# Optimization experiments

Measured on AMD Instinct MI355X. Metric: run time of the kernel, lower is better.

The kernel has to match this reference:

```python
import jax, jax.numpy as jnp
import numpy as np

B, D, K = 32, 400, 200
H = 8            # kernel_size (GRU hidden)
LAYERS = 4
OUT = 8


def setup_inputs() -> dict:
    key = jax.random.key(0)
    ks = jax.random.split(key, 16)
    x = jax.random.normal(ks[0], (B, D, K), dtype=jnp.float32)
    # variable-length zero padding along time per (b, k) sequence
    lengths = jax.random.randint(ks[1], (B, K), D // 2, D + 1)
    tmask = jnp.arange(D)[None, :, None] < lengths[:, None, :]   # (B, D, K)
    x = x * tmask
    s = 1.0 / np.sqrt(H)
    def u(k, shape):
        return jax.random.uniform(k, shape, jnp.float32, -s, s)
    return {
        "x": x,
        "w_ih0": u(ks[2], (2, 3 * H, 1)),
        "w_hh0": u(ks[3], (2, 3 * H, H)),
        "b_ih0": u(ks[4], (2, 3 * H)),
        "b_hh0": u(ks[5], (2, 3 * H)),
        "w_ih": u(ks[6], (LAYERS - 1, 2, 3 * H, 2 * H)),
        "w_hh": u(ks[7], (LAYERS - 1, 2, 3 * H, H)),
        "b_ih": u(ks[8], (LAYERS - 1, 2, 3 * H)),
        "b_hh": u(ks[9], (LAYERS - 1, 2, 3 * H)),
        "lin1_w": u(ks[10], (H, 2 * H)),
        "lin1_b": u(ks[11], (H,)),
        "lin2_w": u(ks[12], (OUT, H)),
        "lin2_b": u(ks[13], (OUT,)),
    }


def _gru_dir(x, mask, Wih, Whh, bih, bhh):
    # x: (N, T, in), mask: (N, T) bool -> (N, T, H); zero past each length
    gi = jnp.einsum('nti,gi->tng', x, Wih) + bih          # (T, N, 3H) input gates
    m = mask.T[:, :, None]                                 # (T, N, 1)
    h0 = jnp.zeros((x.shape[0], Whh.shape[1]), x.dtype)
    def step(h, inp):
        gi_t, m_t = inp
        gh = h @ Whh.T + bhh
        ir, iz, inn = jnp.split(gi_t, 3, axis=-1)          # PyTorch gate order r, z, n
        hr, hz, hn = jnp.split(gh, 3, axis=-1)
        r = jax.nn.sigmoid(ir + hr)
        z = jax.nn.sigmoid(iz + hz)
        n = jnp.tanh(inn + r * hn)
        h = jnp.where(m_t, (1.0 - z) * n + z * h, h)
        return h, jnp.where(m_t, h, 0.0)
    _, out = jax.lax.scan(step, h0, (gi, m))
    return out.transpose(1, 0, 2)


def _bidir_gru(x, mask, rev_idx, p):
    Wih, Whh, bih, bhh = p
    fwd = _gru_dir(x, mask, Wih[0], Whh[0], bih[0], bhh[0])
    # backward dir of a packed sequence: reverse within each valid region
    x_rev = jnp.take_along_axis(x, rev_idx[:, :, None], axis=1)
    bwd_rev = _gru_dir(x_rev, mask, Wih[1], Whh[1], bih[1], bhh[1])
    bwd = jnp.take_along_axis(bwd_rev, rev_idx[:, :, None], axis=1)
    bwd = jnp.where(mask[:, :, None], bwd, 0.0)
    return jnp.concatenate([fwd, bwd], axis=-1)


def _forward(x, w_ih0, w_hh0, b_ih0, b_hh0, w_ih, w_hh, b_ih, b_hh,
             lin1_w, lin1_b, lin2_w, lin2_b):
    b, d, k = x.shape
    seq = x.transpose(0, 2, 1).reshape(b * k, d, 1)         # (N, T, 1)
    vals = seq[:, :, 0]
    zm = vals == 0.0
    lengths = jnp.where(zm.any(axis=1), jnp.argmax(zm, axis=1), d)  # (N,)
    mask = jnp.arange(d)[None, :] < lengths[:, None]        # (N, T)
    rev_idx = jnp.clip(lengths[:, None] - 1 - jnp.arange(d)[None, :], 0, d - 1)
    h = _bidir_gru(seq, mask, rev_idx, (w_ih0, w_hh0, b_ih0, b_hh0))
    for l in range(w_ih.shape[0]):                          # layers 1..3
        h = _bidir_gru(h, mask, rev_idx, (w_ih[l], w_hh[l], b_ih[l], b_hh[l]))
    # last valid timestep per sequence (matches argmax-of-all-zero gather)
    last = jnp.take_along_axis(h, (lengths - 1)[:, None, None], axis=1)[:, 0, :]
    feat = last.reshape(b, k, -1)                           # (B, K, 2H)
    y = jax.nn.leaky_relu(feat @ lin1_w.T + lin1_b, negative_slope=0.2)
    return y @ lin2_w.T + lin2_b                            # (B, K, OUT)


def reference(x, w_ih0, w_hh0, b_ih0, b_hh0, w_ih, w_hh, b_ih, b_hh,
              lin1_w, lin1_b, lin2_w, lin2_b):
    return _forward(x, w_ih0, w_hh0, b_ih0, b_hh0, w_ih, w_hh, b_ih, b_hh,
                    lin1_w, lin1_b, lin2_w, lin2_b)
```

## Files before the change

kernel.cpp:

```cpp
#include <hip/hip_runtime.h>

#define BB 32
#define DD 400
#define KK 200
#define NN (BB*KK)
#define NBINS 512
#define NSIMD 1024

typedef _Float16 half_t;
typedef _Float16 f16x2 __attribute__((ext_vector_type(2)));

__device__ __forceinline__ float dot2(f16x2 w, f16x2 v, float acc) {
  return __builtin_amdgcn_fdot2(w, v, acc, false);
}
__device__ __forceinline__ f16x2 bc16(int v) { return __builtin_bit_cast(f16x2, v); }
__device__ __forceinline__ int pkh(float a, float b) {
  return __builtin_bit_cast(int, __builtin_amdgcn_cvt_pkrtz(a, b));
}

__device__ __forceinline__ float fast_sigmoid(float x) {
  float e = __builtin_amdgcn_exp2f(-1.4426950408889634f * x);
  return __builtin_amdgcn_rcpf(1.0f + e);
}
__device__ __forceinline__ float fast_tanh(float x) {
  float e = __builtin_amdgcn_exp2f(-2.8853900817779268f * x);
  return 2.0f * __builtin_amdgcn_rcpf(1.0f + e) - 1.0f;
}

#define QPERMI(v, P) __builtin_amdgcn_mov_dpp((v), (P)*0x55, 0xF, 0xF, true)
#define HMIRROR(v) __int_as_float(__builtin_amdgcn_mov_dpp(__float_as_int(v), 0x141, 0xF, 0xF, true))

__global__ __launch_bounds__(256) void transpose_x(const float* __restrict__ x,
                                                   float* __restrict__ xt) {
  __shared__ float tile[32][33];
  int b = blockIdx.x, t0 = blockIdx.y * 32, k0 = blockIdx.z * 32;
  int tx = threadIdx.x, ty = threadIdx.y;
#pragma unroll
  for (int i = 0; i < 32; i += 8) {
    int t = t0 + ty + i, k = k0 + tx;
    tile[ty + i][tx] = (t < DD && k < KK) ? x[((size_t)b * DD + t) * KK + k] : 0.0f;
  }
  __syncthreads();
#pragma unroll
  for (int i = 0; i < 32; i += 8) {
    int k = k0 + ty + i, t = t0 + tx;
    if (k < KK && t < DD) xt[((size_t)b * KK + k) * DD + t] = tile[tx][ty + i];
  }
}

__global__ __launch_bounds__(64) void compute_lengths(const float* __restrict__ xt,
                                                      int* __restrict__ lengths,
                                                      int* __restrict__ hist) {
  int n = blockIdx.x, lane = threadIdx.x;
  int m = DD;
  for (int t = lane; t < DD; t += 64) {
    if (xt[(size_t)n * DD + t] == 0.0f) { m = t; break; }
  }
#pragma unroll
  for (int off = 1; off < 64; off <<= 1) {
    int o = __shfl_xor(m, off, 64);
    m = (o < m) ? o : m;
  }
  if (lane == 0) {
    lengths[n] = m;
    atomicAdd(&hist[m], 1);
  }
}

__global__ __launch_bounds__(64) void scan_offsets(const int* __restrict__ hist,
                                                   int* __restrict__ offs) {
  int lane = threadIdx.x;
  int v[8], tot = 0;
#pragma unroll
  for (int i = 0; i < 8; ++i) { v[i] = tot; tot += hist[lane * 8 + i]; }
  int incl = tot;
#pragma unroll
  for (int off = 1; off < 64; off <<= 1) {
    int oth = __shfl_up(incl, off, 64);
    if (lane >= off) incl += oth;
  }
  int excl = incl - tot;
#pragma unroll
  for (int i = 0; i < 8; ++i) offs[lane * 8 + i] = excl + v[i];
}

__global__ __launch_bounds__(256) void scatter_sort(const int* __restrict__ lengths,
                                                    int* __restrict__ offs,
                                                    int* __restrict__ order,
                                                    int* __restrict__ len_sorted) {
  int n = blockIdx.x * 256 + threadIdx.x;
  if (n >= NN) return;
  int len = lengths[n];
  int pos = atomicAdd(&offs[len], 1);
  order[pos] = n;
  len_sorted[pos] = len;
}

__device__ __forceinline__ int octet_of_wave(int p, int W) {
  int E = W - NSIMD;
  if (E <= 0) return W - 1 - p;
  if (p >= NSIMD) return p - NSIMD;
  if (p >= E) return W - 1 - (p - E);
  return (W - 1 - NSIMD + E) - p;
}


template <int IN_DIM, bool IND_IN, bool WRITE_SEQ, bool FWD_ONLY>
__global__ __attribute__((amdgpu_waves_per_eu(2, 2))) __launch_bounds__(64)
void gru_scan(
    const void* __restrict__ in, half_t* __restrict__ out, float* __restrict__ feat,
    const int* __restrict__ len_sorted, const int* __restrict__ order,
    const float* __restrict__ Wih, const float* __restrict__ Whh,
    const float* __restrict__ bih, const float* __restrict__ bhh, int nseq) {
  int p = blockIdx.x;
  int lane = threadIdx.x & 63;
  int G = FWD_ONLY ? nseq : nseq * 2;
  int W = (G + 7) >> 3;
  if (p >= W) return;
  int o = octet_of_wave(p, W);
  int gidx = o * 8 + (lane >> 3);
  int li = lane & 7;
  if (gidx >= G) return;
  int sg  = FWD_ONLY ? gidx : (gidx >> 1);
  int dir = FWD_ONLY ? 0 : (gidx & 1);
  int len = len_sorted[sg];

  int qb = li & 4;
  int wp[3][4];
  f16x2 wi2[3][8];
  float wi1[3];
  float bs[3], bh2;
#pragma unroll
  for (int gt = 0; gt < 3; ++gt) {
    int row = dir * 24 + gt * 8 + li;
    if constexpr (IN_DIM == 16) {
#pragma unroll
      for (int q = 0; q < 8; ++q) {
        f16x2 w;
        w.x = (half_t)Wih[row * 16 + 2 * q];
        w.y = (half_t)Wih[row * 16 + 2 * q + 1];
        wi2[gt][q] = w;
      }
    } else {
      wi1[gt] = Wih[row];
    }
#pragma unroll
    for (int P = 0; P < 4; ++P)
      wp[gt][P] = pkh(Whh[row * 8 + qb + P], Whh[row * 8 + ((qb + P) ^ 7)]);
    bs[gt] = bih[row] + ((gt < 2) ? bhh[row] : 0.0f);
    if (gt == 2) bh2 = bhh[row];
  }

  int steps = len;
  float h = 0.0f;

  const float* px = nullptr;
  const half_t* pxh = nullptr;
  ptrdiff_t xstep;
  if constexpr (IN_DIM == 1) {
    const float* basep = (const float*)in + (IND_IN ? (size_t)order[sg] * DD : (size_t)sg * DD);
    px = basep + ((dir == 0) ? 0 : (len - 1));
    xstep = (dir == 0) ? 1 : -1;
  } else {
    const half_t* basep = (const half_t*)in + (size_t)(sg >> 2) * DD * 64 + (sg & 3) * 8;
    pxh = basep + (size_t)((dir == 0) ? 0 : (len - 1)) * 64;
    xstep = (dir == 0) ? 64 : -64;
  }

  half_t* pw = nullptr; ptrdiff_t wstep = 0;
  if constexpr (WRITE_SEQ) {
    pw = out + ((size_t)(sg >> 2) * DD + ((dir == 0) ? 0 : (len - 1))) * 64
             + dir * 32 + (sg & 3) * 8 + li;
    wstep = (dir == 0) ? 64 : -64;
  }

  auto core = [&](float a0, float a1, float a2) {
    float hm = HMIRROR(h);
    int hp = pkh(h, hm);
    f16x2 u0 = bc16(QPERMI(hp, 0));
    f16x2 u1 = bc16(QPERMI(hp, 1));
    f16x2 u2 = bc16(QPERMI(hp, 2));
    f16x2 u3 = bc16(QPERMI(hp, 3));

    float c0 = dot2(bc16(wp[0][3]), u3, dot2(bc16(wp[0][2]), u2,
               dot2(bc16(wp[0][1]), u1, dot2(bc16(wp[0][0]), u0, a0))));
    float c1 = dot2(bc16(wp[1][3]), u3, dot2(bc16(wp[1][2]), u2,
               dot2(bc16(wp[1][1]), u1, dot2(bc16(wp[1][0]), u0, a1))));
    float c2 = dot2(bc16(wp[2][3]), u3, dot2(bc16(wp[2][2]), u2,
               dot2(bc16(wp[2][1]), u1, dot2(bc16(wp[2][0]), u0, bh2))));

    float r = fast_sigmoid(c0);
    float z = fast_sigmoid(c1);
    float n = fast_tanh(a2 + r * c2);
    h = z * (h - n) + n;
    if constexpr (WRITE_SEQ) { *pw = (half_t)h; pw += wstep; }
  };

  if constexpr (IN_DIM == 1) {
    float s0_, s1_, s2_, s3_;
    auto ld = [&](float& S_) { S_ = *px; px += xstep; };
    auto st = [&](float& S_, bool pf) {
      float a0 = fmaf(wi1[0], S_, bs[0]);
      float a1 = fmaf(wi1[1], S_, bs[1]);
      float a2 = fmaf(wi1[2], S_, bs[2]);
      if (pf) ld(S_);
      core(a0, a1, a2);
    };
    ld(s0_); ld(s1_); ld(s2_); ld(s3_);
    int t = 0;
    for (; t + 4 <= steps; t += 4) {
      st(s0_, true); st(s1_, true); st(s2_, true); st(s3_, true);
    }
    int rem = steps - t;
    if (rem > 0) st(s0_, false);
    if (rem > 1) st(s1_, false);
    if (rem > 2) st(s2_, false);
  } else {
    uint4 b0_[2], b1_[2], b2_[2], b3_[2];
    auto ld = [&](uint4 (&B_)[2]) {
      const uint4* q4 = reinterpret_cast<const uint4*>(pxh);
      B_[0] = q4[0]; B_[1] = q4[4];
      pxh += xstep;
    };
    auto st = [&](uint4 (&B_)[2], bool pf) {
      float a0 = bs[0], a1 = bs[1], a2 = bs[2];
#pragma unroll
      for (int q = 0; q < 2; ++q) {
        f16x2 p0 = __builtin_bit_cast(f16x2, B_[q].x);
        f16x2 p1 = __builtin_bit_cast(f16x2, B_[q].y);
        f16x2 p2 = __builtin_bit_cast(f16x2, B_[q].z);
        f16x2 p3 = __builtin_bit_cast(f16x2, B_[q].w);
        a0 = dot2(wi2[0][4*q], p0, a0); a0 = dot2(wi2[0][4*q+1], p1, a0);
        a0 = dot2(wi2[0][4*q+2], p2, a0); a0 = dot2(wi2[0][4*q+3], p3, a0);
        a1 = dot2(wi2[1][4*q], p0, a1); a1 = dot2(wi2[1][4*q+1], p1, a1);
        a1 = dot2(wi2[1][4*q+2], p2, a1); a1 = dot2(wi2[1][4*q+3], p3, a1);
        a2 = dot2(wi2[2][4*q], p0, a2); a2 = dot2(wi2[2][4*q+1], p1, a2);
        a2 = dot2(wi2[2][4*q+2], p2, a2); a2 = dot2(wi2[2][4*q+3], p3, a2);
      }
      if (pf) ld(B_);
      core(a0, a1, a2);
    };
    ld(b0_); ld(b1_); ld(b2_); ld(b3_);
    int t = 0;
    for (; t + 4 <= steps; t += 4) {
      st(b0_, true); st(b1_, true); st(b2_, true); st(b3_, true);
    }
    int rem = steps - t;
    if (rem > 0) st(b0_, false);
    if (rem > 1) st(b1_, false);
    if (rem > 2) st(b2_, false);
  }

  if constexpr (!WRITE_SEQ) {
    feat[(size_t)order[sg] * 16 + dir * 8 + li] = h;
  }
}

__global__ __launch_bounds__(256) void bwd_last(
    const half_t* __restrict__ in, float* __restrict__ feat,
    const int* __restrict__ len_sorted, const int* __restrict__ order,
    const float* __restrict__ Wih, const float* __restrict__ bih,
    const float* __restrict__ bhh, int nseq) {
  int tid = blockIdx.x * blockDim.x + threadIdx.x;
  int sg = tid >> 3, li = tid & 7;
  if (sg >= nseq) return;
  int len = len_sorted[sg];
  const half_t* xp = in + ((size_t)(sg >> 2) * DD + (len - 1)) * 64 + (sg & 3) * 8;
  float xv[16];
#pragma unroll
  for (int j = 0; j < 8; ++j) { xv[j] = (float)xp[j]; xv[8 + j] = (float)xp[32 + j]; }
  float a[3], bh[3];
#pragma unroll
  for (int gt = 0; gt < 3; ++gt) {
    int row = 24 + gt * 8 + li;
    const float* wpp = Wih + row * 16;
    float acc = bih[row];
#pragma unroll
    for (int j = 0; j < 16; ++j) acc = fmaf(wpp[j], xv[j], acc);
    a[gt] = acc;
    bh[gt] = bhh[row];
  }
  float r = fast_sigmoid(a[0] + bh[0]);
  float z = fast_sigmoid(a[1] + bh[1]);
  float n = fast_tanh(a[2] + r * bh[2]);
  float h = (1.0f - z) * n;
  feat[(size_t)order[sg] * 16 + 8 + li] = h;
}

__global__ __launch_bounds__(256) void head_kernel(
    const float* __restrict__ feat, const float* __restrict__ w1,
    const float* __restrict__ b1, const float* __restrict__ w2,
    const float* __restrict__ b2, float* __restrict__ out) {
  int n = blockIdx.x * blockDim.x + threadIdx.x;
  if (n >= NN) return;
  float f[16];
  const float4* p = reinterpret_cast<const float4*>(feat + (size_t)n * 16);
#pragma unroll
  for (int q = 0; q < 4; ++q) {
    float4 v = p[q];
    f[4*q] = v.x; f[4*q+1] = v.y; f[4*q+2] = v.z; f[4*q+3] = v.w;
  }
  float y[8];
#pragma unroll
  for (int o = 0; o < 8; ++o) {
    float s = b1[o];
#pragma unroll
    for (int j = 0; j < 16; ++j) s += f[j] * w1[o * 16 + j];
    y[o] = (s > 0.0f) ? s : 0.2f * s;
  }
#pragma unroll
  for (int o2 = 0; o2 < 8; ++o2) {
    float s = b2[o2];
#pragma unroll
    for (int o = 0; o < 8; ++o) s += y[o] * w2[o2 * 8 + o];
    out[(size_t)n * 8 + o2] = s;
  }
}

extern "C" void kernel_launch(void* const* d_in, const int* in_sizes, int n_in,
                              void* d_out, int out_size, void* d_ws, size_t ws_size,
                              hipStream_t stream) {
  const float* x      = (const float*)d_in[0];
  const float* w_ih0  = (const float*)d_in[1];
  const float* w_hh0  = (const float*)d_in[2];
  const float* b_ih0  = (const float*)d_in[3];
  const float* b_hh0  = (const float*)d_in[4];
  const float* w_ih   = (const float*)d_in[5];
  const float* w_hh   = (const float*)d_in[6];
  const float* b_ih   = (const float*)d_in[7];
  const float* b_hh   = (const float*)d_in[8];
  const float* lin1_w = (const float*)d_in[9];
  const float* lin1_b = (const float*)d_in[10];
  const float* lin2_w = (const float*)d_in[11];
  const float* lin2_b = (const float*)d_in[12];
  float* out = (float*)d_out;

  char* ws = (char*)d_ws;
  size_t off = 0;
  auto alloc = [&](size_t bytes) -> void* {
    void* p = ws + off;
    off += (bytes + 255) & ~(size_t)255;
    return p;
  };
  alloc(1024);
  float* xt         = (float*)alloc((size_t)NN * DD * sizeof(float) + 1024);
  int*   lengths    = (int*)  alloc((size_t)NN * sizeof(int));
  int*   hist       = (int*)  alloc(NBINS * sizeof(int));
  int*   offs       = (int*)  alloc(NBINS * sizeof(int));
  int*   order      = (int*)  alloc((size_t)NN * sizeof(int));
  int*   len_sorted = (int*)  alloc((size_t)NN * sizeof(int));
  float* feat       = (float*)alloc((size_t)NN * 16 * sizeof(float));
  size_t base = off;
  size_t per_seq = (size_t)DD * 16 * sizeof(half_t) * 2 + 1024;
  int Nc = NN;
  if (base + (size_t)NN * per_seq + 8192 > ws_size) {
    size_t avail = (ws_size > base + 8192) ? (ws_size - base - 8192) : 0;
    size_t nc = avail / per_seq;
    if (nc < 4) nc = 4;
    if (nc > (size_t)NN) nc = NN;
    Nc = (int)(nc & ~(size_t)3);
  }
  alloc(1024);
  half_t* bufA = (half_t*)alloc((size_t)Nc * DD * 16 * sizeof(half_t) + 1024);
  half_t* bufB = (half_t*)alloc((size_t)Nc * DD * 16 * sizeof(half_t) + 1024);

  hipMemsetAsync(hist, 0, NBINS * sizeof(int), stream);
  dim3 gT(BB, (DD + 31) / 32, (KK + 31) / 32), bT(32, 8, 1);
  hipLaunchKernelGGL(transpose_x, gT, bT, 0, stream, x, xt);
  hipLaunchKernelGGL(compute_lengths, dim3(NN), dim3(64), 0, stream, xt, lengths, hist);
  hipLaunchKernelGGL(scan_offsets, dim3(1), dim3(64), 0, stream, hist, offs);
  hipLaunchKernelGGL(scatter_sort, dim3((NN + 255) / 256), dim3(256), 0, stream,
                     lengths, offs, order, len_sorted);

  for (int s0 = 0; s0 < NN; s0 += Nc) {
    int ns = (NN - s0 < Nc) ? (NN - s0) : Nc;
    int W2 = (ns * 2 + 7) / 8;
    int W1 = (ns + 7) / 8;
    int blk1 = (ns * 8 + 255) / 256;
    gru_scan<1, true, true, false><<<W2, 64, 0, stream>>>(
        (const void*)xt, bufA, nullptr, len_sorted + s0, order + s0,
        w_ih0, w_hh0, b_ih0, b_hh0, ns);
    gru_scan<16, false, true, false><<<W2, 64, 0, stream>>>(
        (const void*)bufA, bufB, nullptr, len_sorted + s0, order + s0,
        w_ih + 0 * 2 * 24 * 16, w_hh + 0 * 2 * 24 * 8,
        b_ih + 0 * 2 * 24, b_hh + 0 * 2 * 24, ns);
    gru_scan<16, false, true, false><<<W2, 64, 0, stream>>>(
        (const void*)bufB, bufA, nullptr, len_sorted + s0, order + s0,
        w_ih + 1 * 2 * 24 * 16, w_hh + 1 * 2 * 24 * 8,
        b_ih + 1 * 2 * 24, b_hh + 1 * 2 * 24, ns);
    gru_scan<16, false, false, true><<<W1, 64, 0, stream>>>(
        (const void*)bufA, nullptr, feat, len_sorted + s0, order + s0,
        w_ih + 2 * 2 * 24 * 16, w_hh + 2 * 2 * 24 * 8,
        b_ih + 2 * 2 * 24, b_hh + 2 * 2 * 24, ns);
    hipLaunchKernelGGL(bwd_last, dim3(blk1), dim3(256), 0, stream,
                       bufA, feat, len_sorted + s0, order + s0,
                       w_ih + 2 * 2 * 24 * 16, b_ih + 2 * 2 * 24, b_hh + 2 * 2 * 24, ns);
  }
  hipLaunchKernelGGL(head_kernel, dim3((NN + 255) / 256), dim3(256), 0, stream,
                     feat, lin1_w, lin1_b, lin2_w, lin2_b, out);
}
```

Measured before the change: 373.5 us.

## Fuse all four GRU layers and last-step backward into one persistent kernel

Replaces the four per-layer gru_scan launches and the bwd_last launch with a single kernel where each wave runs all layers back to back for its sequences. Within a wave, the forward and backward lanes of one sequence exchange intermediate sequences through global buffers, with only a vmcnt wait between layers. This removes the inter-kernel launch gaps and the tail idle time at each layer boundary. The price is that the last layer now occupies a full bidirectional grid where backward lanes do only a single step. Cross-lane visibility of global writes within a wave relies on s_waitcnt rather than a proper barrier.

```diff
diff --git a/kernel.cpp b/kernel.cpp
--- a/kernel.cpp
+++ b/kernel.cpp
@@ -105,26 +105,12 @@
 }
 
 
-template <int IN_DIM, bool IND_IN, bool WRITE_SEQ, bool FWD_ONLY>
-__global__ __attribute__((amdgpu_waves_per_eu(2, 2))) __launch_bounds__(64)
-void gru_scan(
+template <int IN_DIM, bool WRITE_SEQ, bool WRITE_FEAT>
+__device__ __forceinline__ void run_layer(
     const void* __restrict__ in, half_t* __restrict__ out, float* __restrict__ feat,
-    const int* __restrict__ len_sorted, const int* __restrict__ order,
+    int sg, int dir, int li, int len, int ord,
     const float* __restrict__ Wih, const float* __restrict__ Whh,
-    const float* __restrict__ bih, const float* __restrict__ bhh, int nseq) {
-  int p = blockIdx.x;
-  int lane = threadIdx.x & 63;
-  int G = FWD_ONLY ? nseq : nseq * 2;
-  int W = (G + 7) >> 3;
-  if (p >= W) return;
-  int o = octet_of_wave(p, W);
-  int gidx = o * 8 + (lane >> 3);
-  int li = lane & 7;
-  if (gidx >= G) return;
-  int sg  = FWD_ONLY ? gidx : (gidx >> 1);
-  int dir = FWD_ONLY ? 0 : (gidx & 1);
-  int len = len_sorted[sg];
-
+    const float* __restrict__ bih, const float* __restrict__ bhh) {
   int qb = li & 4;
   int wp[3][4];
   f16x2 wi2[3][8];
@@ -158,7 +144,7 @@
   const half_t* pxh = nullptr;
   ptrdiff_t xstep;
   if constexpr (IN_DIM == 1) {
-    const float* basep = (const float*)in + (IND_IN ? (size_t)order[sg] * DD : (size_t)sg * DD);
+    const float* basep = (const float*)in + (size_t)ord * DD;
     px = basep + ((dir == 0) ? 0 : (len - 1));
     xstep = (dir == 0) ? 1 : -1;
   } else {
@@ -251,40 +237,72 @@
     if (rem > 2) st(b2_, false);
   }
 
-  if constexpr (!WRITE_SEQ) {
-    feat[(size_t)order[sg] * 16 + dir * 8 + li] = h;
-  }
-}
-
-__global__ __launch_bounds__(256) void bwd_last(
-    const half_t* __restrict__ in, float* __restrict__ feat,
-    const int* __restrict__ len_sorted, const int* __restrict__ order,
-    const float* __restrict__ Wih, const float* __restrict__ bih,
-    const float* __restrict__ bhh, int nseq) {
-  int tid = blockIdx.x * blockDim.x + threadIdx.x;
-  int sg = tid >> 3, li = tid & 7;
-  if (sg >= nseq) return;
+  if constexpr (WRITE_FEAT) {
+    feat[(size_t)ord * 16 + dir * 8 + li] = h;
+  }
+}
+
+__global__ __attribute__((amdgpu_waves_per_eu(2, 2))) __launch_bounds__(64)
+void gru_fused(const float* __restrict__ xt, half_t* __restrict__ bufA,
+               half_t* __restrict__ bufB, float* __restrict__ feat,
+               const int* __restrict__ len_sorted, const int* __restrict__ order,
+               const float* __restrict__ w_ih0, const float* __restrict__ w_hh0,
+               const float* __restrict__ b_ih0, const float* __restrict__ b_hh0,
+               const float* __restrict__ w_ih, const float* __restrict__ w_hh,
+               const float* __restrict__ b_ih, const float* __restrict__ b_hh,
+               int nseq) {
+  int p = blockIdx.x;
+  int lane = threadIdx.x & 63;
+  int G = nseq * 2;
+  int W = (G + 7) >> 3;
+  if (p >= W) return;
+  int o = octet_of_wave(p, W);
+  int gidx = o * 8 + (lane >> 3);
+  int li = lane & 7;
+  int sg = gidx >> 1, dir = gidx & 1;
   int len = len_sorted[sg];
-  const half_t* xp = in + ((size_t)(sg >> 2) * DD + (len - 1)) * 64 + (sg & 3) * 8;
-  float xv[16];
-#pragma unroll
-  for (int j = 0; j < 8; ++j) { xv[j] = (float)xp[j]; xv[8 + j] = (float)xp[32 + j]; }
-  float a[3], bh[3];
-#pragma unroll
-  for (int gt = 0; gt < 3; ++gt) {
-    int row = 24 + gt * 8 + li;
-    const float* wpp = Wih + row * 16;
-    float acc = bih[row];
-#pragma unroll
-    for (int j = 0; j < 16; ++j) acc = fmaf(wpp[j], xv[j], acc);
-    a[gt] = acc;
-    bh[gt] = bhh[row];
-  }
-  float r = fast_sigmoid(a[0] + bh[0]);
-  float z = fast_sigmoid(a[1] + bh[1]);
-  float n = fast_tanh(a[2] + r * bh[2]);
-  float h = (1.0f - z) * n;
-  feat[(size_t)order[sg] * 16 + 8 + li] = h;
+  int ord = order[sg];
+
+  run_layer<1, true, false>(xt, bufA, nullptr, sg, dir, li, len, ord,
+                            w_ih0, w_hh0, b_ih0, b_hh0);
+  __asm__ volatile("s_waitcnt vmcnt(0)" ::: "memory");
+  run_layer<16, true, false>(bufA, bufB, nullptr, sg, dir, li, len, ord,
+                             w_ih + 0 * 2 * 24 * 16, w_hh + 0 * 2 * 24 * 8,
+                             b_ih + 0 * 2 * 24, b_hh + 0 * 2 * 24);
+  __asm__ volatile("s_waitcnt vmcnt(0)" ::: "memory");
+  run_layer<16, true, false>(bufB, bufA, nullptr, sg, dir, li, len, ord,
+                             w_ih + 1 * 2 * 24 * 16, w_hh + 1 * 2 * 24 * 8,
+                             b_ih + 1 * 2 * 24, b_hh + 1 * 2 * 24);
+  __asm__ volatile("s_waitcnt vmcnt(0)" ::: "memory");
+
+  const float* Wih3 = w_ih + 2 * 2 * 24 * 16;
+  const float* bih3 = b_ih + 2 * 2 * 24;
+  const float* bhh3 = b_hh + 2 * 2 * 24;
+  if (dir == 0) {
+    run_layer<16, false, true>(bufA, nullptr, feat, sg, 0, li, len, ord,
+                               Wih3, w_hh + 2 * 2 * 24 * 8, bih3, bhh3);
+  } else {
+    const half_t* xp = bufA + ((size_t)(sg >> 2) * DD + (len - 1)) * 64 + (sg & 3) * 8;
+    float xv[16];
+#pragma unroll
+    for (int j = 0; j < 8; ++j) { xv[j] = (float)xp[j]; xv[8 + j] = (float)xp[32 + j]; }
+    float a[3], bh[3];
+#pragma unroll
+    for (int gt = 0; gt < 3; ++gt) {
+      int row = 24 + gt * 8 + li;
+      const float* wpp = Wih3 + row * 16;
+      float acc = bih3[row];
+#pragma unroll
+      for (int j = 0; j < 16; ++j) acc = fmaf(wpp[j], xv[j], acc);
+      a[gt] = acc;
+      bh[gt] = bhh3[row];
+    }
+    float r = fast_sigmoid(a[0] + bh[0]);
+    float z = fast_sigmoid(a[1] + bh[1]);
+    float n = fast_tanh(a[2] + r * bh[2]);
+    float h = (1.0f - z) * n;
+    feat[(size_t)ord * 16 + 8 + li] = h;
+  }
 }
 
 __global__ __launch_bounds__(256) void head_kernel(
@@ -375,26 +393,10 @@
   for (int s0 = 0; s0 < NN; s0 += Nc) {
     int ns = (NN - s0 < Nc) ? (NN - s0) : Nc;
     int W2 = (ns * 2 + 7) / 8;
-    int W1 = (ns + 7) / 8;
-    int blk1 = (ns * 8 + 255) / 256;
-    gru_scan<1, true, true, false><<<W2, 64, 0, stream>>>(
-        (const void*)xt, bufA, nullptr, len_sorted + s0, order + s0,
-        w_ih0, w_hh0, b_ih0, b_hh0, ns);
-    gru_scan<16, false, true, false><<<W2, 64, 0, stream>>>(
-        (const void*)bufA, bufB, nullptr, len_sorted + s0, order + s0,
-        w_ih + 0 * 2 * 24 * 16, w_hh + 0 * 2 * 24 * 8,
-        b_ih + 0 * 2 * 24, b_hh + 0 * 2 * 24, ns);
-    gru_scan<16, false, true, false><<<W2, 64, 0, stream>>>(
-        (const void*)bufB, bufA, nullptr, len_sorted + s0, order + s0,
-        w_ih + 1 * 2 * 24 * 16, w_hh + 1 * 2 * 24 * 8,
-        b_ih + 1 * 2 * 24, b_hh + 1 * 2 * 24, ns);
-    gru_scan<16, false, false, true><<<W1, 64, 0, stream>>>(
-        (const void*)bufA, nullptr, feat, len_sorted + s0, order + s0,
-        w_ih + 2 * 2 * 24 * 16, w_hh + 2 * 2 * 24 * 8,
-        b_ih + 2 * 2 * 24, b_hh + 2 * 2 * 24, ns);
-    hipLaunchKernelGGL(bwd_last, dim3(blk1), dim3(256), 0, stream,
-                       bufA, feat, len_sorted + s0, order + s0,
-                       w_ih + 2 * 2 * 24 * 16, b_ih + 2 * 2 * 24, b_hh + 2 * 2 * 24, ns);
+    hipLaunchKernelGGL(gru_fused, dim3(W2), dim3(64), 0, stream,
+                       xt, bufA, bufB, feat, len_sorted + s0, order + s0,
+                       w_ih0, w_hh0, b_ih0, b_hh0,
+                       w_ih, w_hh, b_ih, b_hh, ns);
   }
   hipLaunchKernelGGL(head_kernel, dim3((NN + 255) / 256), dim3(256), 0, stream,
                      feat, lin1_w, lin1_b, lin2_w, lin2_b, out);
```

Result: no change. 380.6 us (+1.9%).
